# Kernel optimization log

Measured on AMD Instinct MI355X. Metric: run time of the kernel, lower is better.

Reference implementation:

```python
import jax, jax.numpy as jnp
import numpy as np

HID = 768
INTER = 3072
H = 12
DH = 64
N = 16384
W = 256   # attention_width
L = 512   # per-sequence length (power of 2, used via the uint32 bit-mask trick)


def rotate_every_two(x):
    x1 = x[..., ::2]
    x2 = x[..., 1::2]
    return jnp.stack((-x2, x1), axis=-1).reshape(x.shape)


def setup_inputs() -> dict:
    key = jax.random.key(0)
    ks = jax.random.split(key, 6)
    # GPT-J style interleaved rotary tables: sin/cos each value repeated twice
    inv_freq = 1.0 / (10000.0 ** (np.arange(0, DH, 2) / DH))  # [DH/2]
    ang = np.arange(N)[:, None] * inv_freq[None, :]           # [N, DH/2]
    pos_sin = jnp.asarray(np.repeat(np.sin(ang), 2, axis=-1), dtype=jnp.float32)
    pos_cos = jnp.asarray(np.repeat(np.cos(ang), 2, axis=-1), dtype=jnp.float32)
    return {
        "x": jax.random.normal(ks[0], (N, HID), dtype=jnp.float32),
        "normed_ages": jax.random.normal(ks[1], (N,), dtype=jnp.float32),
        "pos_sin": pos_sin,
        "pos_cos": pos_cos,
        "ln_scale": jnp.ones((HID,), dtype=jnp.float32),
        "ln_offset": jnp.zeros((HID,), dtype=jnp.float32),
        "w_in": jax.random.normal(ks[2], (HID, 3 * HID + INTER), dtype=jnp.float32) * 0.02,
        "b_in": jnp.zeros((3 * HID + INTER,), dtype=jnp.float32),
        "w_out": jax.random.normal(ks[3], (HID + INTER, HID), dtype=jnp.float32) * 0.02,
        "b_out": jnp.zeros((HID,), dtype=jnp.float32),
        "length": L,
    }


def reference(x, normed_ages, pos_sin, pos_cos, ln_scale, ln_offset,
              w_in, b_in, w_out, b_out, length):
    # LayerNorm (haiku: eps=1e-5, create_scale/offset)
    mu = jnp.mean(x, axis=-1, keepdims=True)
    var = jnp.var(x, axis=-1, keepdims=True)
    xn = (x - mu) * jax.lax.rsqrt(var + 1e-5) * ln_scale + ln_offset

    # fused QKV + FF projection (note: original computes x_with_ages but never uses it)
    mid = xn @ w_in + b_in
    q, k, v, ff = jnp.split(mid, [HID, 2 * HID, 3 * HID], axis=-1)

    def to_heads(t):  # [N, HID] -> [H, N, DH]
        return t.reshape(N, H, DH).transpose(1, 0, 2)

    q, k, v = to_heads(q), to_heads(k), to_heads(v)

    # rotary ('per_head'): sincos broadcast over heads
    sin, cos = pos_sin[None], pos_cos[None]
    q = q * cos + rotate_every_two(q) * sin
    k = k * cos + rotate_every_two(k) * sin

    # local (sliding-window, causal, within-sequence) attention, chunked by W
    C = W
    nc = N // C
    qc = q.reshape(H, nc, C, DH)
    kc = k.reshape(H, nc, C, DH)
    vc = v.reshape(H, nc, C, DH)
    kprev = jnp.concatenate([jnp.zeros_like(kc[:, :1]), kc[:, :-1]], axis=1)
    vprev = jnp.concatenate([jnp.zeros_like(vc[:, :1]), vc[:, :-1]], axis=1)
    kcat = jnp.concatenate([kprev, kc], axis=2)  # [H, nc, 2C, DH]
    vcat = jnp.concatenate([vprev, vc], axis=2)

    qi = (jnp.arange(nc) * C)[:, None] + jnp.arange(C)        # [nc, C]
    kj = (jnp.arange(nc) * C)[:, None] - C + jnp.arange(2 * C)  # [nc, 2C]
    lm = ~(jnp.uint32(length) - jnp.uint32(1))  # same bit-trick as the module
    same_seq = ((qi[:, :, None].astype(jnp.uint32) & lm) ==
                (jnp.maximum(kj, 0)[:, None, :].astype(jnp.uint32) & lm))
    d = qi[:, :, None] - kj[:, None, :]
    mask = (kj[:, None, :] >= 0) & (d >= 0) & (d < W) & same_seq  # [nc, C, 2C]

    scale = 1.0 / jnp.sqrt(jnp.float32(DH))
    scores = jnp.einsum('hncd,hnkd->hnck', qc, kcat) * scale
    scores = jnp.where(mask[None], scores, jnp.float32(-1e30))
    probs = jax.nn.softmax(scores, axis=-1)
    attn = jnp.einsum('hnck,hnkd->hncd', probs, vcat)

    attn = attn.reshape(H, N, DH).transpose(1, 0, 2).reshape(N, HID)
    combined = jnp.concatenate([attn, jax.nn.gelu(ff)], axis=-1)
    return xn + combined @ w_out + b_out
```

## Files before the change

kernel.cpp:

```cpp
#include <hip/hip_runtime.h>

#define N_TOK 16384
#define HIDN  768
#define MIDN  5376
#define COMBN 3840
#define NH    12
#define DHD   64
#define CHUNK 256
#define WIN   256

typedef short s16x8 __attribute__((ext_vector_type(8)));
typedef short s16x4 __attribute__((ext_vector_type(4)));
typedef float f32x4 __attribute__((ext_vector_type(4)));

__device__ __forceinline__ float bf2f(unsigned short u){
  union { unsigned u; float f; } x; x.u = ((unsigned)u) << 16; return x.f;
}
__device__ __forceinline__ unsigned short f2bf(float f){
  union { float f; unsigned u; } x; x.f = f;
  unsigned r = x.u + 0x7fffu + ((x.u >> 16) & 1u);
  return (unsigned short)(r >> 16);
}
__device__ __forceinline__ float gelu_fast(float x){
  float u = -1.5957691216057308f * (x + 0.044715f * x * x * x);
  return x / (1.f + __expf(u));
}
__device__ __forceinline__ void glds16(const void* g, void* l){
  __builtin_amdgcn_global_load_lds(
      (const __attribute__((address_space(1))) unsigned*)g,
      (__attribute__((address_space(3))) unsigned*)l, 16, 0, 0);
}

__global__ __launch_bounds__(256) void transpose_f2b(
    const float* __restrict__ in, unsigned short* __restrict__ out,
    int R, int Cc)
{
  __shared__ short t[64 * 72];
  const int tid = threadIdx.x;
  const int r0 = blockIdx.y * 64, c0 = blockIdx.x * 64;
  #pragma unroll
  for (int rep = 0; rep < 4; rep++){
    int v = tid + 256 * rep;
    int r = v >> 4, s = v & 15;
    float4 d = *(const float4*)(in + (size_t)(r0 + r) * Cc + c0 + s * 4);
    s16x4 o = { (short)f2bf(d.x), (short)f2bf(d.y), (short)f2bf(d.z), (short)f2bf(d.w) };
    *(s16x4*)(t + r * 72 + s * 4) = o;
  }
  __syncthreads();
  #pragma unroll
  for (int rep = 0; rep < 2; rep++){
    int v = tid + 256 * rep;
    int c = v & 63, s2 = v >> 6;
    s16x8 d;
    #pragma unroll
    for (int j = 0; j < 8; j++) d[j] = t[(s2 * 8 + j) * 72 + c];
    *(s16x8*)(out + (size_t)(c0 + c) * R + r0 + s2 * 8) = d;
  }
}

__global__ __launch_bounds__(256) void ln_kernel(
    const float* __restrict__ x, const float* __restrict__ sc,
    const float* __restrict__ ofs, unsigned short* __restrict__ xn)
{
  const int lane = threadIdx.x & 63, wv = threadIdx.x >> 6;
  const int row = blockIdx.x * 4 + wv;
  const float4* xr = (const float4*)(x + (size_t)row * HIDN);
  float4 vals[3];
  float sum = 0.f, sq = 0.f;
  #pragma unroll
  for (int j = 0; j < 3; j++){
    vals[j] = xr[lane + 64 * j];
    sum += vals[j].x + vals[j].y + vals[j].z + vals[j].w;
    sq  += vals[j].x * vals[j].x + vals[j].y * vals[j].y
         + vals[j].z * vals[j].z + vals[j].w * vals[j].w;
  }
  #pragma unroll
  for (int o = 1; o < 64; o <<= 1){ sum += __shfl_xor(sum, o); sq += __shfl_xor(sq, o); }
  const float mu = sum * (1.f / HIDN);
  const float rs = rsqrtf(fmaxf(sq * (1.f / HIDN) - mu * mu, 0.f) + 1e-5f);
  s16x4* xo = (s16x4*)(xn + (size_t)row * HIDN);
  const float4* scp = (const float4*)sc;
  const float4* ofp = (const float4*)ofs;
  #pragma unroll
  for (int j = 0; j < 3; j++){
    int p = lane + 64 * j;
    float4 s = scp[p], o = ofp[p];
    s16x4 w;
    w[0] = (short)f2bf((vals[j].x - mu) * rs * s.x + o.x);
    w[1] = (short)f2bf((vals[j].y - mu) * rs * s.y + o.y);
    w[2] = (short)f2bf((vals[j].z - mu) * rs * s.z + o.z);
    w[3] = (short)f2bf((vals[j].w - mu) * rs * s.w + o.w);
    xo[p] = w;
  }
}

template<int K>
__device__ __forceinline__ void gemm_pipe2(
    const unsigned short* __restrict__ A, const unsigned short* __restrict__ BT,
    short* SM,
    int tid, int quad, int l15, int wr, int wc, int m0, int n0,
    f32x4 acc[4][4])
{
  constexpr int T = K / 64;
  char* const SMc = (char*)SM;
  const int srow = tid >> 2;
  const int ksw  = ((tid & 3) ^ ((tid >> 3) & 3)) * 8;
  const unsigned short* Ap = A  + (size_t)(m0 + srow) * K + ksw;
  const unsigned short* Bp = BT + (size_t)(n0 + srow) * K + ksw;
  const size_t rstep = (size_t)64 * K;

  const int segx = ((quad ^ ((l15 >> 1) & 3)) << 4);
  int offA[4], offB[4];
  #pragma unroll
  for (int mf = 0; mf < 4; mf++) offA[mf] = (wr * 64 + mf * 16 + l15) * 64 + segx;
  #pragma unroll
  for (int nf = 0; nf < 4; nf++) offB[nf] = (wc * 64 + nf * 16 + l15) * 64 + segx;

  auto stage = [&](int tt, int kh, int b){
    const int coff = tt * 64 + kh * 32;
    char* Ad = SMc + b * 32768 + kh * 8192 + tid * 16;
    char* Bd = SMc + b * 32768 + 16384 + kh * 8192 + tid * 16;
    glds16(Ap + coff,         Ad);
    glds16(Ap + coff + rstep, Ad + 4096);
    glds16(Bp + coff,         Bd);
    glds16(Bp + coff + rstep, Bd + 4096);
  };

  s16x8 af[4], bf[4];
  auto rdfrags = [&](int b, int kh){
    const char* Ab = SMc + b * 32768 + kh * 8192;
    const char* Bb = SMc + b * 32768 + 16384 + kh * 8192;
    #pragma unroll
    for (int i = 0; i < 4; i++) af[i] = *(const s16x8*)(Ab + offA[i]);
    #pragma unroll
    for (int j = 0; j < 4; j++) bf[j] = *(const s16x8*)(Bb + offB[j]);
  };

  stage(0, 0, 0);
  stage(0, 1, 0);
  asm volatile("s_waitcnt vmcnt(4)" ::: "memory");
  asm volatile("s_barrier" ::: "memory");
  rdfrags(0, 0);

  for (int t = 0; t < T; ++t){
    const int cur = t & 1;
    if (t + 1 < T) stage(t + 1, 0, cur ^ 1);
    __builtin_amdgcn_s_setprio(1);
    #pragma unroll
    for (int i = 0; i < 4; i++)
      #pragma unroll
      for (int j = 0; j < 4; j++)
        acc[i][j] = __builtin_amdgcn_mfma_f32_16x16x32_bf16(af[i], bf[j], acc[i][j], 0, 0, 0);
    __builtin_amdgcn_s_setprio(0);
    if (t + 1 < T){ asm volatile("s_waitcnt vmcnt(4)" ::: "memory"); }
    else          { asm volatile("s_waitcnt vmcnt(0)" ::: "memory"); }
    asm volatile("s_barrier" ::: "memory");
    rdfrags(cur, 1);
    if (t + 1 < T) stage(t + 1, 1, cur ^ 1);
    __builtin_amdgcn_s_setprio(1);
    #pragma unroll
    for (int i = 0; i < 4; i++)
      #pragma unroll
      for (int j = 0; j < 4; j++)
        acc[i][j] = __builtin_amdgcn_mfma_f32_16x16x32_bf16(af[i], bf[j], acc[i][j], 0, 0, 0);
    __builtin_amdgcn_s_setprio(0);
    if (t + 1 < T){
      asm volatile("s_waitcnt vmcnt(4)" ::: "memory");
      asm volatile("s_barrier" ::: "memory");
      rdfrags(cur ^ 1, 0);
    }
  }
}

__global__ __launch_bounds__(256, 2) void gemm1_k(
    const unsigned short* __restrict__ A, const unsigned short* __restrict__ BT,
    const float* __restrict__ bias,
    const float* __restrict__ psin, const float* __restrict__ pcos,
    unsigned short* __restrict__ qb, unsigned short* __restrict__ kb,
    unsigned short* __restrict__ vb, unsigned short* __restrict__ comb)
{
  __shared__ short SM[32768];
  const int tid = threadIdx.x, lane = tid & 63, wv = tid >> 6;
  const int quad = lane >> 4, l15 = lane & 15;
  const int wr = wv >> 1, wc = wv & 1;

  const int p = blockIdx.x + blockIdx.y * gridDim.x;
  const int xcd = p & 7, slot = p >> 3;
  const int m0 = (xcd * 16 + (slot & 15)) * 128;
  const int n0 = (slot >> 4) * 128;

  f32x4 acc[4][4];
  #pragma unroll
  for (int i = 0; i < 4; i++)
    #pragma unroll
    for (int j = 0; j < 4; j++) acc[i][j] = (f32x4){0.f,0.f,0.f,0.f};

  gemm_pipe2<HIDN>(A, BT, SM, tid, quad, l15, wr, wc, m0, n0, acc);

  unsigned short* dstb; int cb; int cls;
  if (n0 < 768)       { dstb = qb;   cb = n0;        cls = 0; }
  else if (n0 < 1536) { dstb = kb;   cb = n0 - 768;  cls = 1; }
  else if (n0 < 2304) { dstb = vb;   cb = n0 - 1536; cls = 2; }
  else                { dstb = comb; cb = n0 - 1536; cls = 3; }
  const int rowstride = (cls == 3) ? COMBN : HIDN;

  float bsv[4];
  #pragma unroll
  for (int nf = 0; nf < 4; nf++) bsv[nf] = bias[n0 + wc * 64 + nf * 16 + l15];

  if (cls <= 1){
    const float qscale = (cls == 0) ? 0.125f : 1.0f;
    #pragma unroll
    for (int mf = 0; mf < 4; mf++){
      #pragma unroll
      for (int r = 0; r < 4; r++){
        const int row = m0 + wr * 64 + mf * 16 + quad * 4 + r;
        unsigned short* rp = dstb + (size_t)row * rowstride + cb + wc * 64;
        const float* sp = psin + (size_t)row * DHD;
        const float* cp = pcos + (size_t)row * DHD;
        #pragma unroll
        for (int nf = 0; nf < 4; nf++){
          const int d = nf * 16 + l15;
          float v = acc[mf][nf][r] + bsv[nf];
          float vp = __shfl_xor(v, 1);
          const float s = sp[d], c = cp[d];
          float o = (l15 & 1) ? (v * c + vp * s) : (v * c - vp * s);
          rp[d] = f2bf(o * qscale);
        }
      }
    }
  } else {
    #pragma unroll
    for (int mf = 0; mf < 4; mf++){
      #pragma unroll
      for (int r = 0; r < 4; r++){
        const int row = m0 + wr * 64 + mf * 16 + quad * 4 + r;
        unsigned short* rp = dstb + (size_t)row * rowstride + cb + wc * 64;
        #pragma unroll
        for (int nf = 0; nf < 4; nf++){
          float val = acc[mf][nf][r] + bsv[nf];
          if (cls == 3) val = gelu_fast(val);
          rp[nf * 16 + l15] = f2bf(val);
        }
      }
    }
  }
}

__global__ __launch_bounds__(256, 2) void gemm2_k(
    const unsigned short* __restrict__ A, const unsigned short* __restrict__ BT,
    const float* __restrict__ bias, const unsigned short* __restrict__ xn,
    float* __restrict__ outp)
{
  __shared__ short SM[32768];
  const int tid = threadIdx.x, lane = tid & 63, wv = tid >> 6;
  const int quad = lane >> 4, l15 = lane & 15;
  const int wr = wv >> 1, wc = wv & 1;
  const int n0 = blockIdx.x * 128, m0 = blockIdx.y * 128;

  f32x4 acc[4][4];
  #pragma unroll
  for (int i = 0; i < 4; i++)
    #pragma unroll
    for (int j = 0; j < 4; j++) acc[i][j] = (f32x4){0.f,0.f,0.f,0.f};

  gemm_pipe2<COMBN>(A, BT, SM, tid, quad, l15, wr, wc, m0, n0, acc);

  float bsv[4];
  #pragma unroll
  for (int nf = 0; nf < 4; nf++) bsv[nf] = bias[n0 + wc * 64 + nf * 16 + l15];

  #pragma unroll
  for (int mf = 0; mf < 4; mf++){
    #pragma unroll
    for (int r = 0; r < 4; r++){
      const int row = m0 + wr * 64 + mf * 16 + quad * 4 + r;
      const size_t rb = (size_t)row * HIDN + n0 + wc * 64;
      #pragma unroll
      for (int nf = 0; nf < 4; nf++){
        const size_t o = rb + nf * 16 + l15;
        outp[o] = bf2f(xn[o]) + acc[mf][nf][r] + bsv[nf];
      }
    }
  }
}

__global__ __launch_bounds__(256) void attn_kernel(
    const unsigned short* __restrict__ qb, const unsigned short* __restrict__ kb,
    const unsigned short* __restrict__ vb, unsigned short* __restrict__ comb,
    const int* __restrict__ lenp)
{
  __shared__ short Ks[2][64 * 72];
  __shared__ short Vt[2][64 * 64];
  __shared__ short Ps[4][16 * 72];
  const int tid = threadIdx.x, lane = tid & 63, wv = tid >> 6;
  const int quad = lane >> 4, l15 = lane & 15;
  const int h = blockIdx.y, c = blockIdx.x;
  const unsigned lm = ~((unsigned)lenp[0] - 1u);
  const int i0 = c * CHUNK + wv * 64;
  const unsigned short* qh = qb + h * DHD;
  const unsigned short* kh = kb + h * DHD;
  const unsigned short* vh = vb + h * DHD;

  s16x8 qf[4][2];
  #pragma unroll
  for (int rt = 0; rt < 4; rt++){
    const unsigned short* qr = qh + (size_t)(i0 + rt * 16 + l15) * HIDN;
    qf[rt][0] = *(const s16x8*)(qr + quad * 8);
    qf[rt][1] = *(const s16x8*)(qr + 32 + quad * 8);
  }

  f32x4 O[4][4];
  float mm[4][4], ll[4][4];
  #pragma unroll
  for (int rt = 0; rt < 4; rt++)
    #pragma unroll
    for (int j = 0; j < 4; j++){ O[rt][j] = (f32x4){0,0,0,0}; mm[rt][j] = -1e30f; ll[rt][j] = 0.f; }
  short* myP = &Ps[wv][0];

  const int skey = tid & 63, sseg = tid >> 6;
  const int jb0 = c * CHUNK - 256;
  s16x8 kr[2], vr[2];

  auto issue = [&](int jb){
    if (jb >= 0){
      const unsigned short* kp = kh + (size_t)(jb + skey) * HIDN + sseg * 16;
      const unsigned short* vp = vh + (size_t)(jb + skey) * HIDN + sseg * 16;
      kr[0] = *(const s16x8*)(kp);     kr[1] = *(const s16x8*)(kp + 8);
      vr[0] = *(const s16x8*)(vp);     vr[1] = *(const s16x8*)(vp + 8);
    } else {
      kr[0] = kr[1] = vr[0] = vr[1] = (s16x8){0,0,0,0,0,0,0,0};
    }
  };

  issue(jb0);
  for (int tb = 0; tb < 8; tb++){
    const int jb = jb0 + tb * 64;
    const int buf = tb & 1;
    short* Kb = &Ks[buf][0];
    short* Vb = &Vt[buf][0];
    *(s16x8*)(Kb + skey * 72 + sseg * 16)     = kr[0];
    *(s16x8*)(Kb + skey * 72 + sseg * 16 + 8) = kr[1];
    #pragma unroll
    for (int half = 0; half < 2; half++)
      #pragma unroll
      for (int j = 0; j < 8; j++){
        const int d = sseg * 16 + half * 8 + j;
        Vb[d * 64 + (((skey & 56) ^ ((d & 7) << 3)) | (skey & 7))] = vr[half][j];
      }
    if (tb < 7) issue(jb + 64);
    __syncthreads();

    const bool act = (jb >= 0) && (jb <= i0 + 63) && (jb + 63 >= i0 - 255) &&
                     (((unsigned)i0 & lm) == ((unsigned)jb & lm));
    if (!act) continue;

    #pragma unroll
    for (int rt = 0; rt < 4; rt++){
      const int ilo = i0 + rt * 16;
      if (ilo + 15 < jb || ilo - (jb + 63) >= WIN) continue;
      f32x4 sc[4];
      #pragma unroll
      for (int ct = 0; ct < 4; ct++){
        const short* kbase = Kb + (ct * 16 + l15) * 72 + quad * 8;
        const s16x8 b0 = *(const s16x8*)(kbase);
        const s16x8 b1 = *(const s16x8*)(kbase + 32);
        f32x4 aa = (f32x4){0,0,0,0};
        aa = __builtin_amdgcn_mfma_f32_16x16x32_bf16(qf[rt][0], b0, aa, 0, 0, 0);
        aa = __builtin_amdgcn_mfma_f32_16x16x32_bf16(qf[rt][1], b1, aa, 0, 0, 0);
        sc[ct] = aa;
      }
      float alph[4];
      #pragma unroll
      for (int r = 0; r < 4; r++){
        const int i = ilo + quad * 4 + r;
        #pragma unroll
        for (int ct = 0; ct < 4; ct++){
          const unsigned dd = (unsigned)(i - (jb + ct * 16 + l15));
          if (dd >= 256u) sc[ct][r] = -1e30f;
        }
        float mx = fmaxf(fmaxf(sc[0][r], sc[1][r]), fmaxf(sc[2][r], sc[3][r]));
        mx = fmaxf(mx, __shfl_xor(mx, 1));
        mx = fmaxf(mx, __shfl_xor(mx, 2));
        mx = fmaxf(mx, __shfl_xor(mx, 4));
        mx = fmaxf(mx, __shfl_xor(mx, 8));
        const float mnew = fmaxf(mm[rt][r], mx);
        alph[r] = __expf(mm[rt][r] - mnew);
        mm[rt][r] = mnew;
        float p0 = __expf(sc[0][r] - mnew);
        float p1 = __expf(sc[1][r] - mnew);
        float p2 = __expf(sc[2][r] - mnew);
        float p3 = __expf(sc[3][r] - mnew);
        sc[0][r] = p0; sc[1][r] = p1; sc[2][r] = p2; sc[3][r] = p3;
        float rsum = (p0 + p1) + (p2 + p3);
        rsum += __shfl_xor(rsum, 1);
        rsum += __shfl_xor(rsum, 2);
        rsum += __shfl_xor(rsum, 4);
        rsum += __shfl_xor(rsum, 8);
        ll[rt][r] = ll[rt][r] * alph[r] + rsum;
      }
      #pragma unroll
      for (int co = 0; co < 4; co++)
        #pragma unroll
        for (int r = 0; r < 4; r++) O[rt][co][r] *= alph[r];
      #pragma unroll
      for (int r = 0; r < 4; r++){
        const int prow = quad * 4 + r;
        #pragma unroll
        for (int ct = 0; ct < 4; ct++)
          myP[prow * 72 + ct * 16 + l15] = (short)f2bf(sc[ct][r]);
      }
      #pragma unroll
      for (int ks2 = 0; ks2 < 2; ks2++){
        const s16x8 pf = *(const s16x8*)(myP + l15 * 72 + ks2 * 32 + quad * 8);
        #pragma unroll
        for (int co = 0; co < 4; co++){
          const int d = co * 16 + l15;
          const s16x8 vf = *(const s16x8*)(Vb + d * 64 +
                              ((ks2 * 32 + quad * 8) ^ ((d & 7) << 3)));
          O[rt][co] = __builtin_amdgcn_mfma_f32_16x16x32_bf16(pf, vf, O[rt][co], 0, 0, 0);
        }
      }
    }
  }

  #pragma unroll
  for (int rt = 0; rt < 4; rt++)
    #pragma unroll
    for (int co = 0; co < 4; co++)
      #pragma unroll
      for (int r = 0; r < 4; r++){
        const int tok = i0 + rt * 16 + quad * 4 + r;
        comb[(size_t)tok * COMBN + h * DHD + co * 16 + l15] = f2bf(O[rt][co][r] / ll[rt][r]);
      }
}

extern "C" void kernel_launch(void* const* d_in, const int* in_sizes, int n_in,
                              void* d_out, int out_size, void* d_ws, size_t ws_size,
                              hipStream_t stream)
{
  const float* x     = (const float*)d_in[0];
  const float* psin  = (const float*)d_in[2];
  const float* pcos  = (const float*)d_in[3];
  const float* lns   = (const float*)d_in[4];
  const float* lno   = (const float*)d_in[5];
  const float* w_in  = (const float*)d_in[6];
  const float* b_in  = (const float*)d_in[7];
  const float* w_out = (const float*)d_in[8];
  const float* b_out = (const float*)d_in[9];
  const int*   lenp  = (const int*)d_in[10];
  float* out = (float*)d_out;

  char* ws = (char*)d_ws;
  size_t off = 0;
  unsigned short* xn    = (unsigned short*)(ws + off); off += (size_t)N_TOK * HIDN * 2;
  unsigned short* wInT  = (unsigned short*)(ws + off); off += (size_t)MIDN * HIDN * 2;
  unsigned short* wOutT = (unsigned short*)(ws + off); off += (size_t)HIDN * COMBN * 2;
  unsigned short* qbuf  = (unsigned short*)(ws + off); off += (size_t)N_TOK * HIDN * 2;
  unsigned short* kbuf  = (unsigned short*)(ws + off); off += (size_t)N_TOK * HIDN * 2;
  unsigned short* vbuf  = (unsigned short*)(ws + off); off += (size_t)N_TOK * HIDN * 2;
  unsigned short* comb  = (unsigned short*)(ws + off); off += (size_t)N_TOK * COMBN * 2;

  transpose_f2b<<<dim3(MIDN/64, HIDN/64), 256, 0, stream>>>(w_in, wInT, HIDN, MIDN);
  transpose_f2b<<<dim3(HIDN/64, COMBN/64), 256, 0, stream>>>(w_out, wOutT, COMBN, HIDN);
  ln_kernel<<<dim3(N_TOK/4), 256, 0, stream>>>(x, lns, lno, xn);
  gemm1_k<<<dim3(MIDN/128, N_TOK/128), 256, 0, stream>>>(
      xn, wInT, b_in, psin, pcos, qbuf, kbuf, vbuf, comb);
  attn_kernel<<<dim3(N_TOK/CHUNK, NH), 256, 0, stream>>>(
      qbuf, kbuf, vbuf, comb, lenp);
  gemm2_k<<<dim3(HIDN/128, N_TOK/128), 256, 0, stream>>>(
      comb, wOutT, b_out, xn, out);
}
```

Measured before the change: 608.2 us.

## Deepen GEMM pipeline to four K32 stages and regroup gemm1 block mapping

```diff
diff --git a/kernel.cpp b/kernel.cpp
--- a/kernel.cpp
+++ b/kernel.cpp
@@ -95,19 +95,19 @@
 }
 
 template<int K>
-__device__ __forceinline__ void gemm_pipe2(
+__device__ __forceinline__ void gemm_pipe3(
     const unsigned short* __restrict__ A, const unsigned short* __restrict__ BT,
     short* SM,
     int tid, int quad, int l15, int wr, int wc, int m0, int n0,
     f32x4 acc[4][4])
 {
-  constexpr int T = K / 64;
+  constexpr int T = K / 32;
   char* const SMc = (char*)SM;
   const int srow = tid >> 2;
   const int ksw  = ((tid & 3) ^ ((tid >> 3) & 3)) * 8;
   const unsigned short* Ap = A  + (size_t)(m0 + srow) * K + ksw;
   const unsigned short* Bp = BT + (size_t)(n0 + srow) * K + ksw;
-  const size_t rstep = (size_t)64 * K;
+  const size_t hstep = (size_t)64 * K;
 
   const int segx = ((quad ^ ((l15 >> 1) & 3)) << 4);
   int offA[4], offB[4];
@@ -116,47 +116,34 @@
   #pragma unroll
   for (int nf = 0; nf < 4; nf++) offB[nf] = (wc * 64 + nf * 16 + l15) * 64 + segx;
 
-  auto stage = [&](int tt, int kh, int b){
-    const int coff = tt * 64 + kh * 32;
-    char* Ad = SMc + b * 32768 + kh * 8192 + tid * 16;
-    char* Bd = SMc + b * 32768 + 16384 + kh * 8192 + tid * 16;
-    glds16(Ap + coff,         Ad);
-    glds16(Ap + coff + rstep, Ad + 4096);
-    glds16(Bp + coff,         Bd);
-    glds16(Bp + coff + rstep, Bd + 4096);
+  auto stage = [&](int tt){
+    const int b = tt & 3;
+    char* Ad = SMc + b * 16384 + tid * 16;
+    char* Bd = SMc + b * 16384 + 8192 + tid * 16;
+    glds16(Ap + tt * 32,         Ad);
+    glds16(Ap + tt * 32 + hstep, Ad + 4096);
+    glds16(Bp + tt * 32,         Bd);
+    glds16(Bp + tt * 32 + hstep, Bd + 4096);
   };
 
   s16x8 af[4], bf[4];
-  auto rdfrags = [&](int b, int kh){
-    const char* Ab = SMc + b * 32768 + kh * 8192;
-    const char* Bb = SMc + b * 32768 + 16384 + kh * 8192;
+  auto rdfrags = [&](int b){
+    const char* Ab = SMc + b * 16384;
+    const char* Bb = SMc + b * 16384 + 8192;
     #pragma unroll
     for (int i = 0; i < 4; i++) af[i] = *(const s16x8*)(Ab + offA[i]);
     #pragma unroll
     for (int j = 0; j < 4; j++) bf[j] = *(const s16x8*)(Bb + offB[j]);
   };
 
-  stage(0, 0, 0);
-  stage(0, 1, 0);
-  asm volatile("s_waitcnt vmcnt(4)" ::: "memory");
+  stage(0); stage(1); stage(2); stage(3);
+  asm volatile("s_waitcnt vmcnt(12)" ::: "memory");
   asm volatile("s_barrier" ::: "memory");
-  rdfrags(0, 0);
-
+  rdfrags(0);
+
+  #pragma unroll 4
   for (int t = 0; t < T; ++t){
-    const int cur = t & 1;
-    if (t + 1 < T) stage(t + 1, 0, cur ^ 1);
-    __builtin_amdgcn_s_setprio(1);
-    #pragma unroll
-    for (int i = 0; i < 4; i++)
-      #pragma unroll
-      for (int j = 0; j < 4; j++)
-        acc[i][j] = __builtin_amdgcn_mfma_f32_16x16x32_bf16(af[i], bf[j], acc[i][j], 0, 0, 0);
-    __builtin_amdgcn_s_setprio(0);
-    if (t + 1 < T){ asm volatile("s_waitcnt vmcnt(4)" ::: "memory"); }
-    else          { asm volatile("s_waitcnt vmcnt(0)" ::: "memory"); }
-    asm volatile("s_barrier" ::: "memory");
-    rdfrags(cur, 1);
-    if (t + 1 < T) stage(t + 1, 1, cur ^ 1);
+    if (t + 4 < T) stage(t + 4);
     __builtin_amdgcn_s_setprio(1);
     #pragma unroll
     for (int i = 0; i < 4; i++)
@@ -165,9 +152,12 @@
         acc[i][j] = __builtin_amdgcn_mfma_f32_16x16x32_bf16(af[i], bf[j], acc[i][j], 0, 0, 0);
     __builtin_amdgcn_s_setprio(0);
     if (t + 1 < T){
-      asm volatile("s_waitcnt vmcnt(4)" ::: "memory");
+      if (t + 4 < T)      { asm volatile("s_waitcnt vmcnt(12)" ::: "memory"); }
+      else if (t + 3 < T) { asm volatile("s_waitcnt vmcnt(8)"  ::: "memory"); }
+      else if (t + 2 < T) { asm volatile("s_waitcnt vmcnt(4)"  ::: "memory"); }
+      else                { asm volatile("s_waitcnt vmcnt(0)"  ::: "memory"); }
       asm volatile("s_barrier" ::: "memory");
-      rdfrags(cur ^ 1, 0);
+      rdfrags((t + 1) & 3);
     }
   }
 }
@@ -184,10 +174,13 @@
   const int quad = lane >> 4, l15 = lane & 15;
   const int wr = wv >> 1, wc = wv & 1;
 
-  const int p = blockIdx.x + blockIdx.y * gridDim.x;
-  const int xcd = p & 7, slot = p >> 3;
-  const int m0 = (xcd * 16 + (slot & 15)) * 128;
-  const int n0 = (slot >> 4) * 128;
+  const int nbx = gridDim.x;
+  const int bid = blockIdx.x + blockIdx.y * nbx;
+  const int GM = 16;
+  const int group = bid / (GM * nbx);
+  const int rem   = bid % (GM * nbx);
+  const int m0 = (group * GM + (rem % GM)) * 128;
+  const int n0 = (rem / GM) * 128;
 
   f32x4 acc[4][4];
   #pragma unroll
@@ -195,7 +188,7 @@
     #pragma unroll
     for (int j = 0; j < 4; j++) acc[i][j] = (f32x4){0.f,0.f,0.f,0.f};
 
-  gemm_pipe2<HIDN>(A, BT, SM, tid, quad, l15, wr, wc, m0, n0, acc);
+  gemm_pipe3<HIDN>(A, BT, SM, tid, quad, l15, wr, wc, m0, n0, acc);
 
   unsigned short* dstb; int cb; int cls;
   if (n0 < 768)       { dstb = qb;   cb = n0;        cls = 0; }
@@ -264,7 +257,7 @@
     #pragma unroll
     for (int j = 0; j < 4; j++) acc[i][j] = (f32x4){0.f,0.f,0.f,0.f};
 
-  gemm_pipe2<COMBN>(A, BT, SM, tid, quad, l15, wr, wc, m0, n0, acc);
+  gemm_pipe3<COMBN>(A, BT, SM, tid, quad, l15, wr, wc, m0, n0, acc);
 
   float bsv[4];
   #pragma unroll
```

Result: no change. 608.4 us (+0.0%).
